# Kernel tuning notes

Measured on AMD Instinct MI355X. Metric: run time of the kernel, lower is better.

## Reference

```python
import jax, jax.numpy as jnp
import numpy as np

WS = 14            # window height/width
CLS = 1            # cls tokens
DIM = 768
H = 12             # heads
DH = DIM // H      # head dim = 64
B = 128
N = WS * WS + CLS  # 197
SCALE = DH ** (-0.5)
TABLE = (2 * WS - 1) ** 2 + CLS  # 730


def _rel_index():
    # Swin-style relative position index, with CLS rows/cols pointing at the
    # last table entry (torch uses index -1 which wraps to TABLE-1).
    c = np.arange(WS)
    coords = np.stack(np.meshgrid(c, c, indexing='ij'))      # [2,14,14]
    cf = coords.reshape(2, -1)                                # [2,196]
    rel = cf[:, :, None] - cf[:, None, :]                     # [2,196,196]
    rel = rel.transpose(1, 2, 0).astype(np.int64)             # [196,196,2]
    rel[..., 0] += WS - 1
    rel[..., 1] += WS - 1
    rel[..., 0] *= 2 * WS - 1
    idx = rel.sum(-1)                                         # [196,196]
    full = np.full((N, N), -1, np.int64)
    full[CLS:, CLS:] = idx
    full = np.where(full < 0, TABLE - 1, full)
    return jnp.asarray(full, jnp.int32)


def setup_inputs() -> dict:
    key = jax.random.key(0)
    ks = jax.random.split(key, 5)
    return {
        'x': jax.random.normal(ks[0], (B, N, DIM), jnp.float32),
        'qkv_w': jax.random.normal(ks[1], (3 * DIM, DIM), jnp.float32) * 0.02,
        'proj_w': jax.random.normal(ks[2], (DIM, DIM), jnp.float32) * 0.02,
        'proj_b': jnp.zeros((DIM,), jnp.float32),
        'bias_table': jax.random.normal(ks[3], (TABLE, H), jnp.float32) * 0.02,
        'rel_idx': _rel_index(),
    }


def reference(x, qkv_w, proj_w, proj_b, bias_table, rel_idx):
    Bc, Nc, C = x.shape
    qkv = x @ qkv_w.T                                   # [B,N,3C]
    qkv = qkv.reshape(Bc, Nc, 3, H, DH).transpose(2, 0, 3, 1, 4)
    q, k, v = qkv[0], qkv[1], qkv[2]                    # [B,H,N,D]
    attn = jnp.einsum('bhnd,bhmd->bhnm', q, k) * SCALE  # [B,H,N,N]
    bias = bias_table[rel_idx]                          # [N,N,H]
    attn = attn + bias.transpose(2, 0, 1)[None]         # broadcast over batch
    attn = jax.nn.softmax(attn, axis=-1)
    out = jnp.einsum('bhnm,bhmd->bhnd', attn, v)        # [B,H,N,D]
    out = out.transpose(0, 2, 1, 3).reshape(Bc, Nc, C)
    return out @ proj_w.T + proj_b
```

## Files before the change

kernel.cpp:

```cpp
#include <hip/hip_runtime.h>
#include <hip/hip_bf16.h>

typedef _Float16 half8 __attribute__((ext_vector_type(8)));
typedef _Float16 half4 __attribute__((ext_vector_type(4)));
typedef float floatx4 __attribute__((ext_vector_type(4)));

#define MFMA16(a, b, c) __builtin_amdgcn_mfma_f32_16x16x32_f16(a, b, c, 0, 0, 0)
#define GLDS16(gp, lp) __builtin_amdgcn_global_load_lds( \
    (const __attribute__((address_space(1))) void*)(gp), \
    (__attribute__((address_space(3))) void*)(lp), 16, 0, 0)

#define BATCH 128
#define NTOK 197
#define NPAD 208
#define DIM 768
#define NH 12
#define DH 64
#define M_ROWS (BATCH * NTOK)
#define MP_ROWS (BATCH * NPAD)
#define KPAD 224
#define NKT 13

#define PREP_X (MP_ROWS * (DIM / 8))
#define PREP_WQ (3 * DIM * DIM / 8)
#define PREP_WP (DIM * DIM / 8)
#define PREP_B (NH * 13 * 13 * 256)
#define PREP_VZ (BATCH * NH * DH * 2)
#define PREP_TOT (PREP_X + PREP_WQ + PREP_WP + PREP_B + PREP_VZ)

#define BAR() __asm__ volatile("s_barrier" ::: "memory")
#define VMW4() __asm__ volatile("s_waitcnt vmcnt(4)" ::: "memory")
#define VMW0() __asm__ volatile("s_waitcnt vmcnt(0)" ::: "memory")

#define STG(gp, lp) do { \
    GLDS16((gp), (lp)); \
    GLDS16((gp) + 64 * DIM, (lp) + 4096); } while (0)

__device__ __forceinline__ half8 cvt8(const float* s) {
    float4 v0 = *(const float4*)s;
    float4 v1 = *(const float4*)(s + 4);
    half8 o;
    o[0] = (_Float16)v0.x; o[1] = (_Float16)v0.y;
    o[2] = (_Float16)v0.z; o[3] = (_Float16)v0.w;
    o[4] = (_Float16)v1.x; o[5] = (_Float16)v1.y;
    o[6] = (_Float16)v1.z; o[7] = (_Float16)v1.w;
    return o;
}

__global__ void prep_kernel(const float* __restrict__ x,
                            const float* __restrict__ qkv_w,
                            const float* __restrict__ proj_w,
                            const float* __restrict__ table,
                            const int* __restrict__ ridx,
                            _Float16* __restrict__ xh,
                            _Float16* __restrict__ wqkvh,
                            _Float16* __restrict__ wprojh,
                            _Float16* __restrict__ biasph,
                            _Float16* __restrict__ vt) {
    int idx = blockIdx.x * 256 + threadIdx.x;
    if (idx < PREP_X) {
        int row = idx / (DIM / 8), ch = idx - row * (DIM / 8);
        int b = row / NPAD, n = row - b * NPAD;
        half8 o = {};
        if (n < NTOK) o = cvt8(x + (size_t)(b * NTOK + n) * DIM + ch * 8);
        *(half8*)&xh[(size_t)row * DIM + ch * 8] = o;
        return;
    }
    idx -= PREP_X;
    if (idx < PREP_WQ) {
        *(half8*)&wqkvh[idx * 8] = cvt8(qkv_w + idx * 8);
        return;
    }
    idx -= PREP_WQ;
    if (idx < PREP_WP) {
        *(half8*)&wprojh[idx * 8] = cvt8(proj_w + idx * 8);
        return;
    }
    idx -= PREP_WP;
    if (idx < PREP_B) {
        int e = idx & 255;
        int r = e >> 4, q = (e >> 2) & 3, rr = e & 3;
        int t = idx >> 8;
        int nt = t % 13; int t2 = t / 13; int qt = t2 % 13; int h = t2 / 13;
        int row = qt * 16 + q * 4 + rr;
        int col = nt * 16 + r;
        float v = -30000.0f;
        if (col < NTOK) {
            int rc = row < NTOK ? row : NTOK - 1;
            v = table[ridx[rc * NTOK + col] * NH + h];
        }
        biasph[idx] = (_Float16)v;
        return;
    }
    idx -= PREP_B;
    if (idx < PREP_VZ) {
        int row = idx >> 1, c = idx & 1;
        half8 z = {};
        *(half8*)&vt[(size_t)row * KPAD + 208 + c * 8] = z;
    }
}

template <int VM, bool SA, bool SB>
__device__ __forceinline__ void qkv_tile(int t, _Float16* smem,
                                         const _Float16* ga0, const _Float16* ga1,
                                         const _Float16* gb0, const _Float16* gb1,
                                         int sbase, int r, int q, int wm, int wn,
                                         floatx4 (&acc)[8][4]) {
    const int buf = t & 1;
    const int r7 = r & 7;
    const int sl0 = (q ^ r7) * 8;
    const int sl1 = sl0 ^ 32;
    _Float16* base = smem + buf * 32768;
    const _Float16* Ab = base + wm * 8192 + r * 64;
    const _Float16* Bb = base + 16384 + (wn >> 1) * 8192 + ((wn & 1) * 64 + r) * 64;
    _Float16* sA0 = smem + (buf ^ 1) * 32768 + sbase;
    _Float16* sA1 = sA0 + 8192;
    _Float16* sB0 = base + 16384 + sbase;
    _Float16* sB1 = sB0 + 8192;
    const int kof1 = (t + 1) * 64, kof2 = (t + 2) * 64;

    half8 a[4][2], b[4][2];

#pragma unroll
    for (int i = 0; i < 4; ++i) {
        a[i][0] = *(const half8*)(Ab + i * 1024 + sl0);
        a[i][1] = *(const half8*)(Ab + i * 1024 + sl1);
    }
#pragma unroll
    for (int j = 0; j < 4; ++j) {
        b[j][0] = *(const half8*)(Bb + j * 1024 + sl0);
        b[j][1] = *(const half8*)(Bb + j * 1024 + sl1);
    }
    if (SA) { STG(ga0 + kof1, sA0); STG(ga1 + kof1, sA1); }
    __builtin_amdgcn_s_setprio(1);
#pragma unroll
    for (int s = 0; s < 2; ++s)
#pragma unroll
        for (int i = 0; i < 4; ++i)
#pragma unroll
            for (int j = 0; j < 4; ++j)
                acc[i][j] = MFMA16(a[i][s], b[j][s], acc[i][j]);
    __builtin_amdgcn_s_setprio(0);
    BAR();

#pragma unroll
    for (int i = 0; i < 4; ++i) {
        a[i][0] = *(const half8*)(Ab + (4 + i) * 1024 + sl0);
        a[i][1] = *(const half8*)(Ab + (4 + i) * 1024 + sl1);
    }
    if (SB) { STG(gb0 + kof2, sB0); STG(gb1 + kof2, sB1); }
    __builtin_amdgcn_s_setprio(1);
#pragma unroll
    for (int s = 0; s < 2; ++s)
#pragma unroll
        for (int i = 0; i < 4; ++i)
#pragma unroll
            for (int j = 0; j < 4; ++j)
                acc[4 + i][j] = MFMA16(a[i][s], b[j][s], acc[4 + i][j]);
    __builtin_amdgcn_s_setprio(0);
    if (VM == 4) { VMW4(); }
    else if (VM == 0) { VMW0(); }
    BAR();
}

__global__ __launch_bounds__(512, 2) void qkv_gemm8(const _Float16* __restrict__ X,
                                                    const _Float16* __restrict__ W,
                                                    _Float16* __restrict__ qh,
                                                    _Float16* __restrict__ kh,
                                                    _Float16* __restrict__ vt) {
    __shared__ __align__(16) _Float16 smem[65536];
    const int tid = threadIdx.x;
    const int lane = tid & 63, wid = tid >> 6;
    const int r = lane & 15, q = lane >> 4;
    const int wm = wid >> 2, wn = wid & 3;

    const int id = blockIdx.x;
    const int swz = (id & 7) * 117 + (id >> 3);
    const int by = swz / 9, bx = swz - by * 9;
    const int m0b = by * 256, n0b = bx * 256;

    const int srow = wid * 8 + (lane >> 3);
    const int sch = (lane & 7) ^ (lane >> 3);
    const _Float16* ga0 = X + (size_t)(m0b + srow) * DIM + sch * 8;
    const _Float16* ga1 = ga0 + (size_t)128 * DIM;
    const _Float16* gb0 = W + (size_t)(n0b + srow) * DIM + sch * 8;
    const _Float16* gb1 = gb0 + (size_t)128 * DIM;
    const int sbase = wid * 512;

    floatx4 acc[8][4] = {};

    STG(ga0, smem + sbase);
    STG(ga1, smem + 8192 + sbase);
    STG(gb0, smem + 16384 + sbase);
    STG(gb1, smem + 24576 + sbase);
    STG(gb0 + 64, smem + 32768 + 16384 + sbase);
    STG(gb1 + 64, smem + 32768 + 24576 + sbase);
    VMW4();
    BAR();

#pragma unroll 2
    for (int t = 0; t < 10; ++t)
        qkv_tile<4, true, true>(t, smem, ga0, ga1, gb0, gb1, sbase, r, q, wm, wn, acc);
    qkv_tile<0, true, false>(10, smem, ga0, ga1, gb0, gb1, sbase, r, q, wm, wn, acc);
    qkv_tile<-1, false, false>(11, smem, ga0, ga1, gb0, gb1, sbase, r, q, wm, wn, acc);

    __syncthreads();
    const int which = bx / 3;
    const int cb = (bx - which * 3) * 256;
    if (which == 2) {
#pragma unroll
        for (int hp = 0; hp < 2; ++hp) {
            if (wm == hp) {
#pragma unroll
                for (int i = 0; i < 8; ++i)
#pragma unroll
                    for (int j = 0; j < 4; ++j) {
                        half4 hv;
#pragma unroll
                        for (int rr = 0; rr < 4; ++rr) hv[rr] = (_Float16)acc[i][j][rr];
                        *(half4*)&smem[(wn * 64 + j * 16 + r) * 136 + i * 16 + q * 4] = hv;
                    }
            }
            __syncthreads();
#pragma unroll
            for (int p = 0; p < 8; ++p) {
                int idx = p * 512 + tid;
                int c = idx >> 4, g0 = (idx & 15) * 8;
                int grow = m0b + hp * 128 + g0;
                int b_idx = grow / NPAD, n_idx = grow - b_idx * NPAD;
                int vcol = cb + c;
                int hh = vcol >> 6, d = vcol & 63;
                half8 hv = *(const half8*)&smem[c * 136 + g0];
                *(half8*)&vt[((size_t)(b_idx * NH + hh) * DH + d) * KPAD + n_idx] = hv;
            }
            __syncthreads();
        }
    } else {
        const float scale = (which == 0) ? 0.125f : 1.0f;
        _Float16* dst = (which == 0) ? qh : kh;
#pragma unroll
        for (int hp = 0; hp < 2; ++hp) {
            if (wm == hp) {
#pragma unroll
                for (int i = 0; i < 8; ++i)
#pragma unroll
                    for (int j = 0; j < 4; ++j)
#pragma unroll
                        for (int rr = 0; rr < 4; ++rr)
                            smem[(i * 16 + q * 4 + rr) * 272 + wn * 64 + j * 16 + r] =
                                (_Float16)(acc[i][j][rr] * scale);
            }
            __syncthreads();
#pragma unroll
            for (int p = 0; p < 8; ++p) {
                int idx = p * 512 + tid;
                int g = idx >> 5, c0 = (idx & 31) * 8;
                int grow = m0b + hp * 128 + g;
                int b_idx = grow / NPAD, n_idx = grow - b_idx * NPAD;
                int colm = cb + c0;
                int hh = colm >> 6, d0 = colm & 63;
                half8 hv = *(const half8*)&smem[g * 272 + c0];
                *(half8*)&dst[((size_t)(b_idx * NH + hh) * NPAD + n_idx) * DH + d0] = hv;
            }
            __syncthreads();
        }
    }
}

__device__ __forceinline__ void gemm_core_768(const _Float16* __restrict__ A,
                                              const _Float16* __restrict__ B,
                                              int m0b, int n0b,
                                              _Float16* As, _Float16* Bs,
                                              floatx4 acc[4][4]) {
    const int lane = threadIdx.x & 63;
    const int w = threadIdx.x >> 6;
    const int r = lane & 15, q = lane >> 4;
    const int mo = (w & 1) * 64;
    const int no = (w >> 1) * 64;
    const int srow = w * 32 + (lane >> 3);
    const int gatom = (lane & 7) ^ (lane >> 3);
    const int rx = r & 7;

    const _Float16* pa[4];
    const _Float16* pb[4];
#pragma unroll
    for (int c = 0; c < 4; ++c) {
        pa[c] = A + (size_t)(m0b + srow + c * 8) * DIM + gatom * 8;
        pb[c] = B + (size_t)(n0b + srow + c * 8) * DIM + gatom * 8;
    }
    _Float16* ldsA = As + w * 2048;
    _Float16* ldsB = Bs + w * 2048;

    for (int kk = 0; kk < DIM / 64; ++kk) {
#pragma unroll
        for (int c = 0; c < 4; ++c) {
            GLDS16(pa[c], ldsA + c * 512);
            GLDS16(pb[c], ldsB + c * 512);
            pa[c] += 64;
            pb[c] += 64;
        }
        __syncthreads();
#pragma unroll
        for (int s = 0; s < 2; ++s) {
            half8 a[4], b[4];
#pragma unroll
            for (int i = 0; i < 4; ++i)
                a[i] = *(const half8*)&As[((mo + i * 16 + r) * 8 + ((s * 4 + q) ^ rx)) * 8];
#pragma unroll
            for (int j = 0; j < 4; ++j)
                b[j] = *(const half8*)&Bs[((no + j * 16 + r) * 8 + ((s * 4 + q) ^ rx)) * 8];
#pragma unroll
            for (int i = 0; i < 4; ++i)
#pragma unroll
                for (int j = 0; j < 4; ++j)
                    acc[i][j] = MFMA16(a[i], b[j], acc[i][j]);
        }
        __syncthreads();
    }
}

__global__ __launch_bounds__(256) void proj_gemm(const _Float16* __restrict__ A,
                                                 const _Float16* __restrict__ W,
                                                 const float* __restrict__ bias,
                                                 float* __restrict__ out) {
    __shared__ __align__(16) _Float16 As[128 * 64];
    __shared__ __align__(16) _Float16 Bs[128 * 64];
    const int lane = threadIdx.x & 63;
    const int w = threadIdx.x >> 6;
    const int r = lane & 15, q = lane >> 4;

    const int id = blockIdx.x;
    const int xcd = id & 7;
    const int lid = id >> 3;
    const int bx = lid % 6;
    const int by = xcd * 25 + lid / 6;
    if (by >= 197) return;
    const int m0b = by * 128;
    const int n0b = bx * 128;

    floatx4 acc[4][4] = {};
    gemm_core_768(A, W, m0b, n0b, As, Bs, acc);

    const int m0 = m0b + (w & 1) * 64;
    const int n0 = n0b + (w >> 1) * 64;
#pragma unroll
    for (int i = 0; i < 4; ++i) {
#pragma unroll
        for (int rr = 0; rr < 4; ++rr) {
            size_t grow = m0 + i * 16 + q * 4 + rr;
#pragma unroll
            for (int j = 0; j < 4; ++j) {
                int gcol = n0 + j * 16 + r;
                out[grow * DIM + gcol] = acc[i][j][rr] + bias[gcol];
            }
        }
    }
}

__global__ __launch_bounds__(832, 7) void attn_kernel(const _Float16* __restrict__ qh,
                                                      const _Float16* __restrict__ kh,
                                                      const _Float16* __restrict__ vt,
                                                      const _Float16* __restrict__ biasph,
                                                      _Float16* __restrict__ ah) {
    __shared__ __align__(16) _Float16 smem[38016];
    _Float16* Ks = smem;
    _Float16* Vs = smem + 13312;
    _Float16* Pb = smem + 29696;
    const int tid = threadIdx.x;
    const int w = tid >> 6, lane = tid & 63;
    const int r = lane & 15, q = lane >> 4;
    const int xr = r & 7;
    const int bh = ((blockIdx.x & 7) * 192) + (blockIdx.x >> 3);
    const int b = bh / NH, h = bh - b * NH;
    const _Float16* Kb = kh + (size_t)bh * NPAD * DH;
    const _Float16* Vtb = vt + (size_t)bh * DH * KPAD;

#pragma unroll
    for (int rd = 0; rd < 2; ++rd) {
        int i = rd * 832 + tid;
        int g = i >> 3;
        int cs = (i & 7) ^ (g & 7);
        GLDS16(Kb + (size_t)g * DH + cs * 8, Ks + (rd * 832 + w * 64) * 8);
    }
#pragma unroll
    for (int rd = 0; rd < 3; ++rd) {
        int j = rd * 832 + tid;
        if (j < 2048) {
            int g = j >> 5;
            int cs = (j & 31) ^ (g & 7);
            if (cs >= 28) cs = 0;
            GLDS16(Vtb + (size_t)g * KPAD + cs * 8, Vs + (rd * 832 + w * 64) * 8);
        }
    }
    __syncthreads();

    const int rowq = w * 16 + r;
    const _Float16* Qb = qh + (size_t)bh * NPAD * DH;
    half8 aq0 = *(const half8*)(Qb + (size_t)rowq * DH + q * 8);
    half8 aq1 = *(const half8*)(Qb + (size_t)rowq * DH + 32 + q * 8);

    const _Float16* bbase = biasph + (((size_t)h * 13 + w) * 13) * 256 + r * 16 + q * 4;
    half4 pvh[NKT + 1];
    float osum[4] = {0.f, 0.f, 0.f, 0.f};
#pragma unroll
    for (int nt = 0; nt < NKT; ++nt) {
        half4 bv = *(const half4*)(bbase + nt * 256);
        floatx4 acc;
        acc[0] = (float)bv[0]; acc[1] = (float)bv[1];
        acc[2] = (float)bv[2]; acc[3] = (float)bv[3];
        const _Float16* kr = Ks + (nt * 16 + r) * 64;
        half8 b0 = *(const half8*)(kr + (q ^ xr) * 8);
        half8 b1 = *(const half8*)(kr + ((q ^ xr) ^ 4) * 8);
        acc = MFMA16(aq0, b0, acc);
        acc = MFMA16(aq1, b1, acc);
        half4 e4;
#pragma unroll
        for (int rr = 0; rr < 4; ++rr) {
            float e = __expf(acc[rr]);
            osum[rr] += e;
            e4[rr] = (_Float16)e;
        }
        pvh[nt] = e4;
    }
    {
        half4 z = {};
        pvh[NKT] = z;
    }
#pragma unroll
    for (int rr = 0; rr < 4; ++rr) {
#pragma unroll
        for (int m = 1; m <= 8; m <<= 1) osum[rr] += __shfl_xor(osum[rr], m, 64);
    }

    floatx4 oacc[4] = {};
    _Float16* Pw = Pb + w * 640;
#pragma unroll
    for (int kt = 0; kt < 7; ++kt) {
#pragma unroll
        for (int rr = 0; rr < 4; ++rr) {
            Pw[(q * 4 + rr) * 40 + r] = pvh[kt * 2][rr];
            Pw[(q * 4 + rr) * 40 + 16 + r] = pvh[kt * 2 + 1][rr];
        }
        __asm__ volatile("" ::: "memory");
        half8 ap = *(const half8*)&Pw[r * 40 + q * 8];
        __asm__ volatile("" ::: "memory");
#pragma unroll
        for (int dt = 0; dt < 4; ++dt) {
            half8 bv = *(const half8*)(Vs + (dt * 16 + r) * 256 + (((kt * 4 + q) ^ xr) * 8));
            oacc[dt] = MFMA16(ap, bv, oacc[dt]);
        }
    }

#pragma unroll
    for (int rr = 0; rr < 4; ++rr) {
        int row = w * 16 + q * 4 + rr;
        if (row < NTOK) {
            float inv = 1.0f / osum[rr];
            size_t o = ((size_t)b * NTOK + row) * DIM + h * DH;
#pragma unroll
            for (int dt = 0; dt < 4; ++dt)
                ah[o + dt * 16 + r] = (_Float16)(oacc[dt][rr] * inv);
        }
    }
}

extern "C" void kernel_launch(void* const* d_in, const int* in_sizes, int n_in,
                              void* d_out, int out_size, void* d_ws, size_t ws_size,
                              hipStream_t stream) {
    const float* x = (const float*)d_in[0];
    const float* qkv_w = (const float*)d_in[1];
    const float* proj_w = (const float*)d_in[2];
    const float* proj_b = (const float*)d_in[3];
    const float* table = (const float*)d_in[4];
    const int* ridx = (const int*)d_in[5];
    float* out = (float*)d_out;

    char* ws = (char*)d_ws;
    const size_t SZ_XP = (size_t)MP_ROWS * DIM * 2;
    const size_t SZ_WQKV = (size_t)3 * DIM * DIM * 2;
    const size_t SZ_WPROJ = (size_t)DIM * DIM * 2;
    const size_t SZ_QK = (size_t)BATCH * NH * NPAD * DH * 2;
    const size_t SZ_VT = (size_t)BATCH * NH * DH * KPAD * 2;
    const size_t SZ_BIAS = (size_t)NH * 13 * 13 * 256 * 2;

    _Float16* xh = (_Float16*)(ws + 0);
    _Float16* ah = (_Float16*)(ws + 0);
    _Float16* wqkvh = (_Float16*)(ws + SZ_XP);
    _Float16* wprojh = (_Float16*)(ws + SZ_XP + SZ_WQKV);
    _Float16* qh = (_Float16*)(ws + SZ_XP + SZ_WQKV + SZ_WPROJ);
    _Float16* kh = (_Float16*)(ws + SZ_XP + SZ_WQKV + SZ_WPROJ + SZ_QK);
    _Float16* vt = (_Float16*)(ws + SZ_XP + SZ_WQKV + SZ_WPROJ + 2 * SZ_QK);
    _Float16* biasph = (_Float16*)(ws + SZ_XP + SZ_WQKV + SZ_WPROJ + 2 * SZ_QK + SZ_VT);
    (void)SZ_BIAS; (void)ws_size; (void)n_in; (void)in_sizes; (void)out_size;

    prep_kernel<<<(PREP_TOT + 255) / 256, 256, 0, stream>>>(
        x, qkv_w, proj_w, table, ridx, xh, wqkvh, wprojh, biasph, vt);
    qkv_gemm8<<<936, 512, 0, stream>>>(xh, wqkvh, qh, kh, vt);
    attn_kernel<<<BATCH * NH, 832, 0, stream>>>(qh, kh, vt, biasph, ah);
    proj_gemm<<<1200, 256, 0, stream>>>(ah, wprojh, proj_b, out);
}
```

Baseline: 396.6 us.

## Shrink QKV GEMM tile to 128x256 single-buffered for higher occupancy

The QKV projection GEMM moves from 256x256 tiles with a double-buffered, software-pipelined LDS loop to 128x256 tiles with a simple single-buffered loop that waits for each k-slab before computing. LDS use and accumulator registers drop so more workgroups fit per CU (launch bounds raised to 4), and the grid doubles to 1872 blocks. This trades away the explicit load/compute overlap and adds more A/B reloads per output, relying on occupancy to hide latency instead.

```diff
diff --git a/kernel.cpp b/kernel.cpp
--- a/kernel.cpp
+++ b/kernel.cpp
@@ -29,7 +29,6 @@
 #define PREP_TOT (PREP_X + PREP_WQ + PREP_WP + PREP_B + PREP_VZ)
 
 #define BAR() __asm__ volatile("s_barrier" ::: "memory")
-#define VMW4() __asm__ volatile("s_waitcnt vmcnt(4)" ::: "memory")
 #define VMW0() __asm__ volatile("s_waitcnt vmcnt(0)" ::: "memory")
 
 #define STG(gp, lp) do { \
@@ -100,169 +99,122 @@
     }
 }
 
-template <int VM, bool SA, bool SB>
-__device__ __forceinline__ void qkv_tile(int t, _Float16* smem,
-                                         const _Float16* ga0, const _Float16* ga1,
-                                         const _Float16* gb0, const _Float16* gb1,
-                                         int sbase, int r, int q, int wm, int wn,
-                                         floatx4 (&acc)[8][4]) {
-    const int buf = t & 1;
-    const int r7 = r & 7;
-    const int sl0 = (q ^ r7) * 8;
-    const int sl1 = sl0 ^ 32;
-    _Float16* base = smem + buf * 32768;
-    const _Float16* Ab = base + wm * 8192 + r * 64;
-    const _Float16* Bb = base + 16384 + (wn >> 1) * 8192 + ((wn & 1) * 64 + r) * 64;
-    _Float16* sA0 = smem + (buf ^ 1) * 32768 + sbase;
-    _Float16* sA1 = sA0 + 8192;
-    _Float16* sB0 = base + 16384 + sbase;
-    _Float16* sB1 = sB0 + 8192;
-    const int kof1 = (t + 1) * 64, kof2 = (t + 2) * 64;
-
-    half8 a[4][2], b[4][2];
-
-#pragma unroll
-    for (int i = 0; i < 4; ++i) {
-        a[i][0] = *(const half8*)(Ab + i * 1024 + sl0);
-        a[i][1] = *(const half8*)(Ab + i * 1024 + sl1);
-    }
-#pragma unroll
-    for (int j = 0; j < 4; ++j) {
-        b[j][0] = *(const half8*)(Bb + j * 1024 + sl0);
-        b[j][1] = *(const half8*)(Bb + j * 1024 + sl1);
-    }
-    if (SA) { STG(ga0 + kof1, sA0); STG(ga1 + kof1, sA1); }
-    __builtin_amdgcn_s_setprio(1);
-#pragma unroll
-    for (int s = 0; s < 2; ++s)
-#pragma unroll
-        for (int i = 0; i < 4; ++i)
-#pragma unroll
-            for (int j = 0; j < 4; ++j)
-                acc[i][j] = MFMA16(a[i][s], b[j][s], acc[i][j]);
-    __builtin_amdgcn_s_setprio(0);
-    BAR();
-
-#pragma unroll
-    for (int i = 0; i < 4; ++i) {
-        a[i][0] = *(const half8*)(Ab + (4 + i) * 1024 + sl0);
-        a[i][1] = *(const half8*)(Ab + (4 + i) * 1024 + sl1);
-    }
-    if (SB) { STG(gb0 + kof2, sB0); STG(gb1 + kof2, sB1); }
-    __builtin_amdgcn_s_setprio(1);
-#pragma unroll
-    for (int s = 0; s < 2; ++s)
-#pragma unroll
-        for (int i = 0; i < 4; ++i)
-#pragma unroll
-            for (int j = 0; j < 4; ++j)
-                acc[4 + i][j] = MFMA16(a[i][s], b[j][s], acc[4 + i][j]);
-    __builtin_amdgcn_s_setprio(0);
-    if (VM == 4) { VMW4(); }
-    else if (VM == 0) { VMW0(); }
-    BAR();
-}
-
-__global__ __launch_bounds__(512, 2) void qkv_gemm8(const _Float16* __restrict__ X,
+__global__ __launch_bounds__(512, 4) void qkv_gemm8(const _Float16* __restrict__ X,
                                                     const _Float16* __restrict__ W,
                                                     _Float16* __restrict__ qh,
                                                     _Float16* __restrict__ kh,
                                                     _Float16* __restrict__ vt) {
-    __shared__ __align__(16) _Float16 smem[65536];
+    __shared__ __align__(16) _Float16 smem[34816];
     const int tid = threadIdx.x;
     const int lane = tid & 63, wid = tid >> 6;
     const int r = lane & 15, q = lane >> 4;
     const int wm = wid >> 2, wn = wid & 3;
 
     const int id = blockIdx.x;
-    const int swz = (id & 7) * 117 + (id >> 3);
+    const int swz = (id & 7) * 234 + (id >> 3);
     const int by = swz / 9, bx = swz - by * 9;
-    const int m0b = by * 256, n0b = bx * 256;
+    const int m0b = by * 128, n0b = bx * 256;
 
     const int srow = wid * 8 + (lane >> 3);
     const int sch = (lane & 7) ^ (lane >> 3);
     const _Float16* ga0 = X + (size_t)(m0b + srow) * DIM + sch * 8;
-    const _Float16* ga1 = ga0 + (size_t)128 * DIM;
     const _Float16* gb0 = W + (size_t)(n0b + srow) * DIM + sch * 8;
     const _Float16* gb1 = gb0 + (size_t)128 * DIM;
     const int sbase = wid * 512;
 
-    floatx4 acc[8][4] = {};
-
-    STG(ga0, smem + sbase);
-    STG(ga1, smem + 8192 + sbase);
-    STG(gb0, smem + 16384 + sbase);
-    STG(gb1, smem + 24576 + sbase);
-    STG(gb0 + 64, smem + 32768 + 16384 + sbase);
-    STG(gb1 + 64, smem + 32768 + 24576 + sbase);
-    VMW4();
-    BAR();
-
-#pragma unroll 2
-    for (int t = 0; t < 10; ++t)
-        qkv_tile<4, true, true>(t, smem, ga0, ga1, gb0, gb1, sbase, r, q, wm, wn, acc);
-    qkv_tile<0, true, false>(10, smem, ga0, ga1, gb0, gb1, sbase, r, q, wm, wn, acc);
-    qkv_tile<-1, false, false>(11, smem, ga0, ga1, gb0, gb1, sbase, r, q, wm, wn, acc);
+    const int r7 = r & 7;
+    const int sl0 = (q ^ r7) * 8;
+    const int sl1 = sl0 ^ 32;
+    const _Float16* Ab = smem + wm * 4096 + r * 64;
+    const _Float16* Bb = smem + 8192 + wn * 4096 + r * 64;
+
+    floatx4 acc[4][4] = {};
+
+    for (int t = 0; t < 12; ++t) {
+        BAR();
+        STG(ga0, smem + sbase);
+        STG(gb0, smem + 8192 + sbase);
+        STG(gb1, smem + 16384 + sbase);
+        ga0 += 64; gb0 += 64; gb1 += 64;
+        VMW0();
+        BAR();
+        {
+            half8 a[4], b[4];
+#pragma unroll
+            for (int i = 0; i < 4; ++i) a[i] = *(const half8*)(Ab + i * 1024 + sl0);
+#pragma unroll
+            for (int j = 0; j < 4; ++j) b[j] = *(const half8*)(Bb + j * 1024 + sl0);
+            __builtin_amdgcn_s_setprio(1);
+#pragma unroll
+            for (int i = 0; i < 4; ++i)
+#pragma unroll
+                for (int j = 0; j < 4; ++j)
+                    acc[i][j] = MFMA16(a[i], b[j], acc[i][j]);
+            __builtin_amdgcn_s_setprio(0);
+        }
+        {
+            half8 a[4], b[4];
+#pragma unroll
+            for (int i = 0; i < 4; ++i) a[i] = *(const half8*)(Ab + i * 1024 + sl1);
+#pragma unroll
+            for (int j = 0; j < 4; ++j) b[j] = *(const half8*)(Bb + j * 1024 + sl1);
+            __builtin_amdgcn_s_setprio(1);
+#pragma unroll
+            for (int i = 0; i < 4; ++i)
+#pragma unroll
+                for (int j = 0; j < 4; ++j)
+                    acc[i][j] = MFMA16(a[i], b[j], acc[i][j]);
+            __builtin_amdgcn_s_setprio(0);
+        }
+    }
 
     __syncthreads();
     const int which = bx / 3;
     const int cb = (bx - which * 3) * 256;
     if (which == 2) {
 #pragma unroll
-        for (int hp = 0; hp < 2; ++hp) {
-            if (wm == hp) {
-#pragma unroll
-                for (int i = 0; i < 8; ++i)
-#pragma unroll
-                    for (int j = 0; j < 4; ++j) {
-                        half4 hv;
-#pragma unroll
-                        for (int rr = 0; rr < 4; ++rr) hv[rr] = (_Float16)acc[i][j][rr];
-                        *(half4*)&smem[(wn * 64 + j * 16 + r) * 136 + i * 16 + q * 4] = hv;
-                    }
+        for (int i = 0; i < 4; ++i)
+#pragma unroll
+            for (int j = 0; j < 4; ++j) {
+                half4 hv;
+#pragma unroll
+                for (int rr = 0; rr < 4; ++rr) hv[rr] = (_Float16)acc[i][j][rr];
+                *(half4*)&smem[(wn * 64 + j * 16 + r) * 136 + wm * 64 + i * 16 + q * 4] = hv;
             }
-            __syncthreads();
-#pragma unroll
-            for (int p = 0; p < 8; ++p) {
-                int idx = p * 512 + tid;
-                int c = idx >> 4, g0 = (idx & 15) * 8;
-                int grow = m0b + hp * 128 + g0;
-                int b_idx = grow / NPAD, n_idx = grow - b_idx * NPAD;
-                int vcol = cb + c;
-                int hh = vcol >> 6, d = vcol & 63;
-                half8 hv = *(const half8*)&smem[c * 136 + g0];
-                *(half8*)&vt[((size_t)(b_idx * NH + hh) * DH + d) * KPAD + n_idx] = hv;
-            }
-            __syncthreads();
+        __syncthreads();
+#pragma unroll
+        for (int p = 0; p < 8; ++p) {
+            int idx = p * 512 + tid;
+            int c = idx >> 4, g0 = (idx & 15) * 8;
+            int grow = m0b + g0;
+            int b_idx = grow / NPAD, n_idx = grow - b_idx * NPAD;
+            int vcol = cb + c;
+            int hh = vcol >> 6, d = vcol & 63;
+            half8 hv = *(const half8*)&smem[c * 136 + g0];
+            *(half8*)&vt[((size_t)(b_idx * NH + hh) * DH + d) * KPAD + n_idx] = hv;
         }
     } else {
         const float scale = (which == 0) ? 0.125f : 1.0f;
         _Float16* dst = (which == 0) ? qh : kh;
 #pragma unroll
-        for (int hp = 0; hp < 2; ++hp) {
-            if (wm == hp) {
-#pragma unroll
-                for (int i = 0; i < 8; ++i)
-#pragma unroll
-                    for (int j = 0; j < 4; ++j)
-#pragma unroll
-                        for (int rr = 0; rr < 4; ++rr)
-                            smem[(i * 16 + q * 4 + rr) * 272 + wn * 64 + j * 16 + r] =
-                                (_Float16)(acc[i][j][rr] * scale);
-            }
-            __syncthreads();
-#pragma unroll
-            for (int p = 0; p < 8; ++p) {
-                int idx = p * 512 + tid;
-                int g = idx >> 5, c0 = (idx & 31) * 8;
-                int grow = m0b + hp * 128 + g;
-                int b_idx = grow / NPAD, n_idx = grow - b_idx * NPAD;
-                int colm = cb + c0;
-                int hh = colm >> 6, d0 = colm & 63;
-                half8 hv = *(const half8*)&smem[g * 272 + c0];
-                *(half8*)&dst[((size_t)(b_idx * NH + hh) * NPAD + n_idx) * DH + d0] = hv;
-            }
-            __syncthreads();
+        for (int i = 0; i < 4; ++i)
+#pragma unroll
+            for (int j = 0; j < 4; ++j)
+#pragma unroll
+                for (int rr = 0; rr < 4; ++rr)
+                    smem[(wm * 64 + i * 16 + q * 4 + rr) * 272 + wn * 64 + j * 16 + r] =
+                        (_Float16)(acc[i][j][rr] * scale);
+        __syncthreads();
+#pragma unroll
+        for (int p = 0; p < 8; ++p) {
+            int idx = p * 512 + tid;
+            int g = idx >> 5, c0 = (idx & 31) * 8;
+            int grow = m0b + g;
+            int b_idx = grow / NPAD, n_idx = grow - b_idx * NPAD;
+            int colm = cb + c0;
+            int hh = colm >> 6, d0 = colm & 63;
+            half8 hv = *(const half8*)&smem[g * 272 + c0];
+            *(half8*)&dst[((size_t)(b_idx * NH + hh) * NPAD + n_idx) * DH + d0] = hv;
         }
     }
 }
@@ -495,7 +447,7 @@
 
     prep_kernel<<<(PREP_TOT + 255) / 256, 256, 0, stream>>>(
         x, qkv_w, proj_w, table, ridx, xh, wqkvh, wprojh, biasph, vt);
-    qkv_gemm8<<<936, 512, 0, stream>>>(xh, wqkvh, qh, kh, vt);
+    qkv_gemm8<<<1872, 512, 0, stream>>>(xh, wqkvh, qh, kh, vt);
     attn_kernel<<<BATCH * NH, 832, 0, stream>>>(qh, kh, vt, biasph, ah);
     proj_gemm<<<1200, 256, 0, stream>>>(ah, wprojh, proj_b, out);
 }
```

Result: no change. 392.1 us (-1.1%).
